# Kernel optimization log

Hardware: AMD Instinct MI355X
Metric: run time of the kernel (lower is better)

Reference implementation:

```python
import jax, jax.numpy as jnp
import numpy as np

PAD = 2  # kernel_height // 2 for kernel_height=5


def earth_pad2d(x, ph, pw):
    # circular pad in longitude (last dim), zero pad in latitude (dim 2)
    if pw > 0:
        x = jnp.concatenate([x[..., -pw:], x, x[..., :pw]], axis=-1)
    if ph > 0:
        x = jnp.pad(x, ((0, 0), (0, 0), (ph, ph), (0, 0)))
    return x


def earth_wrap2d(x, w, pad):
    # fold circular overhang of a transposed-conv output back onto width w
    core = x[..., pad:pad + w]
    rw = x.shape[-1] - pad - w  # right overhang (stride-1... here 1)
    core = core.at[..., :rw].add(x[..., pad + w:])
    core = core.at[..., w - pad:].add(x[..., :pad])
    return core


def _conv(x, w, b, stride):
    # torch Conv2d, weight [Cout, Cin, 1, k], VALID padding, stride (1, stride)
    y = jax.lax.conv_general_dilated(x, w, (1, stride), 'VALID',
                                     dimension_numbers=('NCHW', 'OIHW', 'NCHW'))
    return y + b[None, :, None, None]


def _convT(x, w, stride):
    # torch ConvTranspose2d (no bias), weight [Cin, Cout, 1, k], padding 0
    k = w.shape[-1]
    wr = jnp.transpose(jnp.flip(w, axis=(2, 3)), (1, 0, 2, 3))  # -> [Cout, Cin, 1, k]
    return jax.lax.conv_general_dilated(x, wr, (1, 1),
                                        [(0, 0), (k - 1, k - 1)],
                                        lhs_dilation=(1, stride),
                                        dimension_numbers=('NCHW', 'OIHW', 'NCHW'))


def _edge(x, d, p):
    return x[:, :, -p:, :] if d == 1 else x[:, :, :p, :]


def _set_edge(x, d, p, v):
    return x.at[:, :, -p:, :].set(v) if d == 1 else x.at[:, :, :p, :].set(v)


def _forward(strips, wi, wo):
    strips_pad = [earth_pad2d(s, PAD, PAD) for s in strips]
    # center strip inner edges from the adjacent coarser strips (to_inners[0])
    for d in (-1, 1):
        a = _edge(strips[2 + d], -d, PAD)
        a = _convT(a, wi[0], 2)
        a = earth_wrap2d(a, strips[2].shape[3], 2)
        a = earth_pad2d(a, 0, PAD)
        strips_pad[2] = _set_edge(strips_pad[2], d, PAD, a)
    # outer strips: far edge from next coarser (to_inners), near edge from finer (to_outers)
    for mi in (1, 2):
        for d in (-1, 1):
            idx = 2 + d * mi
            sp = strips_pad[idx]
            if mi + 1 <= 2:
                o = _edge(strips[2 + d * (mi + 1)], -d, PAD)
                o = _convT(o, wi[mi], 2)
                o = earth_wrap2d(o, strips[idx].shape[3], 2)
                o = earth_pad2d(o, 0, PAD)
                sp = _set_edge(sp, d, PAD, o)
            en = _edge(strips[2 + d * (mi - 1)], d, PAD)
            en = earth_pad2d(en, 0, 2)
            en = _conv(en, wo[mi - 1][0], wo[mi - 1][1], 2)
            en = earth_pad2d(en, 0, PAD)
            sp = _set_edge(sp, -d, PAD, en)
            strips_pad[idx] = sp
    return tuple(strips_pad)


def setup_inputs():
    key = jax.random.key(0)
    ks = jax.random.split(key, 11)
    B, C, W = 1, 256, 1440
    shapes = [(B, C, 30, W // 4), (B, C, 60, W // 2), (B, C, 180, W),
              (B, C, 60, W // 2), (B, C, 30, W // 4)]
    d = {}
    for i, sh in enumerate(shapes):
        d['s%d' % i] = jax.random.normal(ks[i], sh, dtype=jnp.float32)
    scale = 0.03
    d['wi0'] = jax.random.normal(ks[5], (C, C, 1, 5), dtype=jnp.float32) * scale
    d['wi1'] = jax.random.normal(ks[6], (C, C, 1, 5), dtype=jnp.float32) * scale
    d['wo0'] = jax.random.normal(ks[7], (C, C, 1, 5), dtype=jnp.float32) * scale
    d['bo0'] = jax.random.normal(ks[8], (C,), dtype=jnp.float32) * 0.01
    d['wo1'] = jax.random.normal(ks[9], (C, C, 1, 5), dtype=jnp.float32) * scale
    d['bo1'] = jax.random.normal(ks[10], (C,), dtype=jnp.float32) * 0.01
    return d


def reference(s0, s1, s2, s3, s4, wi0, wi1, wo0, bo0, wo1, bo1):
    return _forward([s0, s1, s2, s3, s4], [wi0, wi1], [(wo0, bo0), (wo1, bo1)])
```

## Files before the change

kernel.cpp:

```cpp
#include <hip/hip_runtime.h>


struct ConvJob {
  const float* x; const float* wt; const float* bias; float* out;
  int Hin, Win, r0, Hout, Wcore, h0, blk_start;
};

struct MegaParams {
  ConvJob j[8];
  const float* in0; const float* in1; const float* in2; const float* in3; const float* in4;
  float* o0; float* o1; float* o2; float* o3; float* o4;
  unsigned* ctr;
};

struct WTParams { const float* src[4]; float* dst[4]; unsigned* ctr; };

__global__ __launch_bounds__(256) void transpose_all_kernel(WTParams p) {
  if (blockIdx.x == 0 && threadIdx.x == 0) *p.ctr = 0u;
  int b = blockIdx.x;
  int which = b / 1280;
  int idx = (b - which * 1280) * 256 + threadIdx.x;
  int oc = idx & 255;
  int q = idx >> 8;
  int k = q % 5;
  int ic = q / 5;
  const float* s = p.src[which];
  float v = (which < 2) ? s[(ic * 256 + oc) * 5 + k] : s[(oc * 256 + ic) * 5 + k];
  p.dst[which][idx] = v;
}

template <int H, int W>
__device__ __forceinline__ void copy_row(const float* __restrict__ in,
                                         float* __restrict__ out, int rl, int lane) {
  int c = rl / H;
  const float* src = in + (size_t)rl * W;
  float* dst = out + (size_t)(rl + c * 4 + 2) * (W + 4);
  for (int w4 = 1 + lane; w4 < W / 4; w4 += 64) {
    const float* q = src + w4 * 4;
    float2 a = *(const float2*)(q - 2);
    float2 b = *(const float2*)(q);
    *(float4*)(dst + w4 * 4) = make_float4(a.x, a.y, b.x, b.y);
  }
  if (lane == 0) {
    float2 E = *(const float2*)(src + W - 2);
    float2 F = *(const float2*)(src);
    float4 v = make_float4(E.x, E.y, F.x, F.y);
    *(float4*)(dst) = v;
    *(float4*)(dst + W) = v;
  }
}

__device__ __forceinline__ void zero_row(const MegaParams& p, int z, int lane) {
  int strip = z >> 9, cr = z & 511, c = cr >> 1, r = cr & 1;
  float* dst = strip ? p.o4 + (size_t)(c * 34 + 32 + r) * 364
                     : p.o0 + (size_t)(c * 34 + r) * 364;
  for (int w4 = lane; w4 < 91; w4 += 64)
    *(float4*)(dst + w4 * 4) = make_float4(0.f, 0.f, 0.f, 0.f);
}

__device__ __forceinline__ void do_row(const MegaParams& p, int gid, int lane) {
  if (gid < 46080)      copy_row<180, 1440>(p.in2, p.o2, gid, lane);
  else if (gid < 61440) copy_row<60, 720>(p.in1, p.o1, gid - 46080, lane);
  else if (gid < 76800) copy_row<60, 720>(p.in3, p.o3, gid - 61440, lane);
  else if (gid < 84480) copy_row<30, 360>(p.in0, p.o0, gid - 76800, lane);
  else if (gid < 92160) copy_row<30, 360>(p.in4, p.o4, gid - 84480, lane);
  else                  zero_row(p, gid - 92160, lane);
}

__device__ __forceinline__ void conv_tr(const ConvJob jb, int local, int t, float* xs) {
  int tile = local >> 1;
  int r = local & 1;
  const int Win = jb.Win;
  const float* xrow = jb.x + ((size_t)(t * jb.Hin + jb.r0 + r)) * Win;
  const float* wt = jb.wt + t;
  const int Wop = jb.Wcore + 4;
  float* orow = jb.out + ((size_t)(t * jb.Hout + jb.h0 + r)) * Wop;

  int m0 = tile * 16;
  int j0 = (m0 >> 1) - 1;
#pragma unroll
  for (int cc = 0; cc < 10; ++cc) {
    int col = j0 + cc;
    col += (col < 0) ? Win : 0;
    col -= (col >= Win) ? Win : 0;
    xs[cc * 256 + t] = xrow[col];
  }
  __syncthreads();
  float acc[16];
#pragma unroll
  for (int i = 0; i < 16; ++i) acc[i] = 0.f;
  float w[20], wn[20];
#pragma unroll
  for (int e = 0; e < 20; ++e) w[e] = wt[e * 256];
  for (int ic0 = 0; ic0 < 256; ic0 += 4) {
    if (ic0 + 4 < 256) {
#pragma unroll
      for (int e = 0; e < 20; ++e) wn[e] = wt[(size_t)((ic0 + 4) * 5 + e) * 256];
    }
#pragma unroll
    for (int cc = 0; cc < 10; ++cc) {
      float4 xq = *(const float4*)&xs[cc * 256 + ic0];
#pragma unroll
      for (int ml = 0; ml < 16; ++ml) {
        int k = ml + 4 - 2 * cc;
        if (k >= 0 && k < 5)
          acc[ml] += w[k] * xq.x + w[5 + k] * xq.y + w[10 + k] * xq.z + w[15 + k] * xq.w;
      }
    }
#pragma unroll
    for (int e = 0; e < 20; ++e) w[e] = wn[e];
  }
#pragma unroll
  for (int i = 0; i < 16; ++i) {
    int g = m0 + i;
    float vv = acc[i];
    orow[2 + g] = vv;
    if (g < 2) orow[jb.Wcore + 2 + g] = vv;
    if (g >= jb.Wcore - 2) orow[g - (jb.Wcore - 2)] = vv;
  }
}

__device__ __forceinline__ void conv_fwd(const ConvJob jb, int local, int t, float* xs) {
  int tile = local >> 1;
  int r = local & 1;
  const int Win = jb.Win;
  const float* xrow = jb.x + ((size_t)(t * jb.Hin + jb.r0 + r)) * Win;
  const float* wt = jb.wt + t;
  const int Wop = jb.Wcore + 4;
  float* orow = jb.out + ((size_t)(t * jb.Hout + jb.h0 + r)) * Wop;

  int u0 = tile * 8;
  int cb = 2 * u0 - 2;
#pragma unroll
  for (int cc = 0; cc < 19; ++cc) {
    int col = cb + cc;
    col += (col < 0) ? Win : 0;
    col -= (col >= Win) ? Win : 0;
    xs[cc * 256 + t] = xrow[col];
  }
  __syncthreads();
  float bv = jb.bias[t];
  float acc[8];
#pragma unroll
  for (int i = 0; i < 8; ++i) acc[i] = bv;
  float w[20], wn[20];
#pragma unroll
  for (int e = 0; e < 20; ++e) w[e] = wt[e * 256];
  for (int ic0 = 0; ic0 < 256; ic0 += 4) {
    if (ic0 + 4 < 256) {
#pragma unroll
      for (int e = 0; e < 20; ++e) wn[e] = wt[(size_t)((ic0 + 4) * 5 + e) * 256];
    }
#pragma unroll
    for (int cc = 0; cc < 19; ++cc) {
      float4 xq = *(const float4*)&xs[cc * 256 + ic0];
#pragma unroll
      for (int i = 0; i < 8; ++i) {
        int k = cc - 2 * i;
        if (k >= 0 && k < 5)
          acc[i] += w[k] * xq.x + w[5 + k] * xq.y + w[10 + k] * xq.z + w[15 + k] * xq.w;
      }
    }
#pragma unroll
    for (int e = 0; e < 20; ++e) w[e] = wn[e];
  }
#pragma unroll
  for (int i = 0; i < 8; ++i) {
    int g = u0 + i;
    float vv = acc[i];
    orow[2 + g] = vv;
    if (g < 2) orow[jb.Wcore + 2 + g] = vv;
    if (g >= jb.Wcore - 2) orow[g - (jb.Wcore - 2)] = vv;
  }
}

__global__ __launch_bounds__(256, 4) void mega_kernel(MegaParams p) {
  __shared__ float xs[19 * 256];
  int bx = blockIdx.x;
  int t = threadIdx.x;
  if (bx < 540) {
    int ji = (bx >= 450) ? 3 : (bx >= 360) ? 2 : (bx >= 180) ? 1 : 0;
    conv_tr(p.j[ji], bx - p.j[ji].blk_start, t, xs);
    __syncthreads();
    int u2 = bx + 540;
    int j2 = (u2 >= 990) ? 7 : (u2 >= 900) ? 6 : (u2 >= 720) ? 5 : 4;
    conv_fwd(p.j[j2], u2 - p.j[j2].blk_start, t, xs);
  }
  int lane = t & 63;
  for (;;) {
    int g = 0;
    if (lane == 0) g = (int)atomicAdd(p.ctr, 1u);
    g = __shfl(g, 0, 64);
    if (g >= 11648) break;
    int base = g * 8;
    for (int r = 0; r < 8; ++r) do_row(p, base + r, lane);
  }
}

extern "C" void kernel_launch(void* const* d_in, const int* in_sizes, int n_in,
                              void* d_out, int out_size, void* d_ws, size_t ws_size,
                              hipStream_t stream) {
  const float* s0 = (const float*)d_in[0];
  const float* s1 = (const float*)d_in[1];
  const float* s2 = (const float*)d_in[2];
  const float* s3 = (const float*)d_in[3];
  const float* s4 = (const float*)d_in[4];
  const float* wi0 = (const float*)d_in[5];
  const float* wi1 = (const float*)d_in[6];
  const float* wo0 = (const float*)d_in[7];
  const float* bo0 = (const float*)d_in[8];
  const float* wo1 = (const float*)d_in[9];
  const float* bo1 = (const float*)d_in[10];

  float* out = (float*)d_out;
  float* out0 = out;
  float* out1 = out + 3168256;
  float* out2 = out + 15030272;
  float* out3 = out + 83048448;
  float* out4 = out + 94910464;

  unsigned* ctr = (unsigned*)d_ws;
  float* wt0 = (float*)d_ws + 16;
  float* wt1 = wt0 + 327680;
  float* wt2 = wt1 + 327680;
  float* wt3 = wt2 + 327680;

  WTParams wp;
  wp.src[0] = wi0; wp.src[1] = wi1; wp.src[2] = wo0; wp.src[3] = wo1;
  wp.dst[0] = wt0; wp.dst[1] = wt1; wp.dst[2] = wt2; wp.dst[3] = wt3;
  wp.ctr = ctr;
  transpose_all_kernel<<<5120, 256, 0, stream>>>(wp);

  MegaParams mp;
  mp.j[0] = {s1, wt0, nullptr, out2,  60,  720,  58, 184, 1440,   0,   0};
  mp.j[1] = {s3, wt0, nullptr, out2,  60,  720,   0, 184, 1440, 182, 180};
  mp.j[2] = {s0, wt1, nullptr, out1,  30,  360,  28,  64,  720,   0, 360};
  mp.j[3] = {s4, wt1, nullptr, out3,  30,  360,   0,  64,  720,  62, 450};
  mp.j[4] = {s2, wt2, bo0,     out1, 180, 1440,   0,  64,  720,  62, 540};
  mp.j[5] = {s2, wt2, bo0,     out3, 180, 1440, 178,  64,  720,   0, 720};
  mp.j[6] = {s1, wt3, bo1,     out0,  60,  720,   0,  34,  360,  32, 900};
  mp.j[7] = {s3, wt3, bo1,     out4,  60,  720,  58,  34,  360,   0, 990};
  mp.in0 = s0; mp.in1 = s1; mp.in2 = s2; mp.in3 = s3; mp.in4 = s4;
  mp.o0 = out0; mp.o1 = out1; mp.o2 = out2; mp.o3 = out3; mp.o4 = out4;
  mp.ctr = ctr;

  mega_kernel<<<1024, 256, 0, stream>>>(mp);
}
```

Before: 361.8 us.

## Split fused mega-kernel into separate conv and copy kernels with static scheduling

Replaces the single persistent mega-kernel, which ran two conv tiles per block and then pulled copy rows through an atomic counter, with two launches. The conv kernel assigns one conv tile per block across 1080 blocks, and the copy kernel walks rows with a static grid-stride loop. The conv inner loop is restructured into a double-buffered weight load over a non-unrolled loop, and the copy loop is unrolled by two. This removes atomic contention and the serial two-conv chain per block. In exchange it adds a launch and loses the overlap between conv compute and the bandwidth-bound copy inside one kernel.

New measurement: 466.1 us. 1.29x slower.

```diff
diff --git a/kernel.cpp b/kernel.cpp
--- a/kernel.cpp
+++ b/kernel.cpp
@@ -5,18 +5,16 @@
   const float* x; const float* wt; const float* bias; float* out;
   int Hin, Win, r0, Hout, Wcore, h0, blk_start;
 };
-
-struct MegaParams {
-  ConvJob j[8];
+struct ConvParams { ConvJob j[8]; };
+
+struct CopyParams {
   const float* in0; const float* in1; const float* in2; const float* in3; const float* in4;
   float* o0; float* o1; float* o2; float* o3; float* o4;
-  unsigned* ctr;
 };
 
-struct WTParams { const float* src[4]; float* dst[4]; unsigned* ctr; };
+struct WTParams { const float* src[4]; float* dst[4]; };
 
 __global__ __launch_bounds__(256) void transpose_all_kernel(WTParams p) {
-  if (blockIdx.x == 0 && threadIdx.x == 0) *p.ctr = 0u;
   int b = blockIdx.x;
   int which = b / 1280;
   int idx = (b - which * 1280) * 256 + threadIdx.x;
@@ -29,45 +27,30 @@
   p.dst[which][idx] = v;
 }
 
-template <int H, int W>
-__device__ __forceinline__ void copy_row(const float* __restrict__ in,
-                                         float* __restrict__ out, int rl, int lane) {
-  int c = rl / H;
-  const float* src = in + (size_t)rl * W;
-  float* dst = out + (size_t)(rl + c * 4 + 2) * (W + 4);
-  for (int w4 = 1 + lane; w4 < W / 4; w4 += 64) {
-    const float* q = src + w4 * 4;
-    float2 a = *(const float2*)(q - 2);
-    float2 b = *(const float2*)(q);
-    *(float4*)(dst + w4 * 4) = make_float4(a.x, a.y, b.x, b.y);
-  }
-  if (lane == 0) {
-    float2 E = *(const float2*)(src + W - 2);
-    float2 F = *(const float2*)(src);
-    float4 v = make_float4(E.x, E.y, F.x, F.y);
-    *(float4*)(dst) = v;
-    *(float4*)(dst + W) = v;
-  }
-}
-
-__device__ __forceinline__ void zero_row(const MegaParams& p, int z, int lane) {
-  int strip = z >> 9, cr = z & 511, c = cr >> 1, r = cr & 1;
-  float* dst = strip ? p.o4 + (size_t)(c * 34 + 32 + r) * 364
-                     : p.o0 + (size_t)(c * 34 + r) * 364;
-  for (int w4 = lane; w4 < 91; w4 += 64)
-    *(float4*)(dst + w4 * 4) = make_float4(0.f, 0.f, 0.f, 0.f);
-}
-
-__device__ __forceinline__ void do_row(const MegaParams& p, int gid, int lane) {
-  if (gid < 46080)      copy_row<180, 1440>(p.in2, p.o2, gid, lane);
-  else if (gid < 61440) copy_row<60, 720>(p.in1, p.o1, gid - 46080, lane);
-  else if (gid < 76800) copy_row<60, 720>(p.in3, p.o3, gid - 61440, lane);
-  else if (gid < 84480) copy_row<30, 360>(p.in0, p.o0, gid - 76800, lane);
-  else if (gid < 92160) copy_row<30, 360>(p.in4, p.o4, gid - 84480, lane);
-  else                  zero_row(p, gid - 92160, lane);
-}
-
-__device__ __forceinline__ void conv_tr(const ConvJob jb, int local, int t, float* xs) {
+
+template <int NOUT, int NCC>
+__device__ __forceinline__ void fma_cols(float* acc, const float* w, const float* xsrow,
+                                         int ic0) {
+#pragma unroll
+  for (int cc = 0; cc < NCC; ++cc) {
+    float4 xq = *(const float4*)&xsrow[cc * 256 + ic0];
+#pragma unroll
+    for (int i = 0; i < NOUT; ++i) {
+      int k = (NOUT == 8) ? (cc - 2 * i) : (i + 4 - 2 * cc);
+      if (k >= 0 && k < 5)
+        acc[i] += w[k] * xq.x + w[5 + k] * xq.y + w[10 + k] * xq.z + w[15 + k] * xq.w;
+    }
+  }
+}
+
+__device__ __forceinline__ void wload(float* wbuf, const float* wt, int ic) {
+#pragma unroll
+  for (int e = 0; e < 20; ++e) wbuf[e] = wt[(size_t)(ic * 5 + e) * 256];
+}
+
+template <int NOUT, int NCC>
+__device__ __forceinline__ void conv_unit(const ConvJob jb, int local, int t, float* xs,
+                                          float bv) {
   int tile = local >> 1;
   int r = local & 1;
   const int Win = jb.Win;
@@ -76,43 +59,36 @@
   const int Wop = jb.Wcore + 4;
   float* orow = jb.out + ((size_t)(t * jb.Hout + jb.h0 + r)) * Wop;
 
-  int m0 = tile * 16;
-  int j0 = (m0 >> 1) - 1;
-#pragma unroll
-  for (int cc = 0; cc < 10; ++cc) {
-    int col = j0 + cc;
+  int base0, ncc;
+  if (NOUT == 8) { base0 = 2 * (tile * 8) - 2; ncc = 19; }
+  else           { base0 = (tile * 16 >> 1) - 1; ncc = 10; }
+#pragma unroll
+  for (int cc = 0; cc < NCC; ++cc) {
+    int col = base0 + cc;
     col += (col < 0) ? Win : 0;
     col -= (col >= Win) ? Win : 0;
     xs[cc * 256 + t] = xrow[col];
   }
   __syncthreads();
-  float acc[16];
-#pragma unroll
-  for (int i = 0; i < 16; ++i) acc[i] = 0.f;
-  float w[20], wn[20];
-#pragma unroll
-  for (int e = 0; e < 20; ++e) w[e] = wt[e * 256];
-  for (int ic0 = 0; ic0 < 256; ic0 += 4) {
-    if (ic0 + 4 < 256) {
-#pragma unroll
-      for (int e = 0; e < 20; ++e) wn[e] = wt[(size_t)((ic0 + 4) * 5 + e) * 256];
-    }
-#pragma unroll
-    for (int cc = 0; cc < 10; ++cc) {
-      float4 xq = *(const float4*)&xs[cc * 256 + ic0];
-#pragma unroll
-      for (int ml = 0; ml < 16; ++ml) {
-        int k = ml + 4 - 2 * cc;
-        if (k >= 0 && k < 5)
-          acc[ml] += w[k] * xq.x + w[5 + k] * xq.y + w[10 + k] * xq.z + w[15 + k] * xq.w;
-      }
-    }
-#pragma unroll
-    for (int e = 0; e < 20; ++e) w[e] = wn[e];
-  }
-#pragma unroll
-  for (int i = 0; i < 16; ++i) {
-    int g = m0 + i;
+
+  float acc[NOUT];
+#pragma unroll
+  for (int i = 0; i < NOUT; ++i) acc[i] = bv;
+
+  float wA[20], wB[20];
+  wload(wA, wt, 0);
+#pragma unroll 1
+  for (int ic0 = 0; ic0 < 256; ic0 += 8) {
+    wload(wB, wt, ic0 + 4);
+    fma_cols<NOUT, NCC>(acc, wA, xs, ic0);
+    if (ic0 + 8 < 256) wload(wA, wt, ic0 + 8);
+    fma_cols<NOUT, NCC>(acc, wB, xs, ic0 + 4);
+  }
+
+  int g0 = (NOUT == 8) ? tile * 8 : tile * 16;
+#pragma unroll
+  for (int i = 0; i < NOUT; ++i) {
+    int g = g0 + i;
     float vv = acc[i];
     orow[2 + g] = vv;
     if (g < 2) orow[jb.Wcore + 2 + g] = vv;
@@ -120,81 +96,77 @@
   }
 }
 
-__device__ __forceinline__ void conv_fwd(const ConvJob jb, int local, int t, float* xs) {
-  int tile = local >> 1;
-  int r = local & 1;
-  const int Win = jb.Win;
-  const float* xrow = jb.x + ((size_t)(t * jb.Hin + jb.r0 + r)) * Win;
-  const float* wt = jb.wt + t;
-  const int Wop = jb.Wcore + 4;
-  float* orow = jb.out + ((size_t)(t * jb.Hout + jb.h0 + r)) * Wop;
-
-  int u0 = tile * 8;
-  int cb = 2 * u0 - 2;
-#pragma unroll
-  for (int cc = 0; cc < 19; ++cc) {
-    int col = cb + cc;
-    col += (col < 0) ? Win : 0;
-    col -= (col >= Win) ? Win : 0;
-    xs[cc * 256 + t] = xrow[col];
-  }
-  __syncthreads();
-  float bv = jb.bias[t];
-  float acc[8];
-#pragma unroll
-  for (int i = 0; i < 8; ++i) acc[i] = bv;
-  float w[20], wn[20];
-#pragma unroll
-  for (int e = 0; e < 20; ++e) w[e] = wt[e * 256];
-  for (int ic0 = 0; ic0 < 256; ic0 += 4) {
-    if (ic0 + 4 < 256) {
-#pragma unroll
-      for (int e = 0; e < 20; ++e) wn[e] = wt[(size_t)((ic0 + 4) * 5 + e) * 256];
-    }
-#pragma unroll
-    for (int cc = 0; cc < 19; ++cc) {
-      float4 xq = *(const float4*)&xs[cc * 256 + ic0];
-#pragma unroll
-      for (int i = 0; i < 8; ++i) {
-        int k = cc - 2 * i;
-        if (k >= 0 && k < 5)
-          acc[i] += w[k] * xq.x + w[5 + k] * xq.y + w[10 + k] * xq.z + w[15 + k] * xq.w;
-      }
-    }
-#pragma unroll
-    for (int e = 0; e < 20; ++e) w[e] = wn[e];
-  }
-#pragma unroll
-  for (int i = 0; i < 8; ++i) {
-    int g = u0 + i;
-    float vv = acc[i];
-    orow[2 + g] = vv;
-    if (g < 2) orow[jb.Wcore + 2 + g] = vv;
-    if (g >= jb.Wcore - 2) orow[g - (jb.Wcore - 2)] = vv;
-  }
-}
-
-__global__ __launch_bounds__(256, 4) void mega_kernel(MegaParams p) {
+__global__ __launch_bounds__(256, 4) void conv_kernel(ConvParams p) {
   __shared__ float xs[19 * 256];
   int bx = blockIdx.x;
   int t = threadIdx.x;
   if (bx < 540) {
     int ji = (bx >= 450) ? 3 : (bx >= 360) ? 2 : (bx >= 180) ? 1 : 0;
-    conv_tr(p.j[ji], bx - p.j[ji].blk_start, t, xs);
-    __syncthreads();
-    int u2 = bx + 540;
+    conv_unit<16, 10>(p.j[ji], bx - p.j[ji].blk_start, t, xs, 0.f);
+  } else {
+    int u2 = bx;
     int j2 = (u2 >= 990) ? 7 : (u2 >= 900) ? 6 : (u2 >= 720) ? 5 : 4;
-    conv_fwd(p.j[j2], u2 - p.j[j2].blk_start, t, xs);
-  }
-  int lane = t & 63;
-  for (;;) {
-    int g = 0;
-    if (lane == 0) g = (int)atomicAdd(p.ctr, 1u);
-    g = __shfl(g, 0, 64);
-    if (g >= 11648) break;
-    int base = g * 8;
-    for (int r = 0; r < 8; ++r) do_row(p, base + r, lane);
-  }
+    conv_unit<8, 19>(p.j[j2], u2 - p.j[j2].blk_start, t, xs, p.j[j2].bias[t]);
+  }
+}
+
+
+__device__ __forceinline__ float4 pack4(float2 a, float2 b) {
+  return make_float4(a.x, a.y, b.x, b.y);
+}
+
+template <int H, int W>
+__device__ __forceinline__ void copy_row(const float* __restrict__ in,
+                                         float* __restrict__ out, int rl, int lane) {
+  constexpr int CORE = W / 4;
+  int c = rl / H;
+  const float* src = in + (size_t)rl * W;
+  float* dst = out + (size_t)(rl + c * 4 + 2) * (W + 4);
+  int w4 = 1 + lane;
+  while (w4 < CORE) {
+    int w4b = w4 + 64;
+    float2 a0 = *(const float2*)(src + w4 * 4 - 2);
+    float2 b0 = *(const float2*)(src + w4 * 4);
+    if (w4b < CORE) {
+      float2 a1 = *(const float2*)(src + w4b * 4 - 2);
+      float2 b1 = *(const float2*)(src + w4b * 4);
+      *(float4*)(dst + w4 * 4) = pack4(a0, b0);
+      *(float4*)(dst + w4b * 4) = pack4(a1, b1);
+    } else {
+      *(float4*)(dst + w4 * 4) = pack4(a0, b0);
+    }
+    w4 += 128;
+  }
+  if (lane == 0) {
+    float2 E = *(const float2*)(src + W - 2);
+    float2 F = *(const float2*)(src);
+    float4 v = pack4(E, F);
+    *(float4*)(dst) = v;
+    *(float4*)(dst + W) = v;
+  }
+}
+
+__device__ __forceinline__ void zero_row(const CopyParams& p, int z, int lane) {
+  int strip = z >> 9, cr = z & 511, c = cr >> 1, r = cr & 1;
+  float* dst = strip ? p.o4 + (size_t)(c * 34 + 32 + r) * 364
+                     : p.o0 + (size_t)(c * 34 + r) * 364;
+  for (int w4 = lane; w4 < 91; w4 += 64)
+    *(float4*)(dst + w4 * 4) = make_float4(0.f, 0.f, 0.f, 0.f);
+}
+
+__device__ __forceinline__ void do_row(const CopyParams& p, int gid, int lane) {
+  if (gid < 46080)      copy_row<180, 1440>(p.in2, p.o2, gid, lane);
+  else if (gid < 61440) copy_row<60, 720>(p.in1, p.o1, gid - 46080, lane);
+  else if (gid < 76800) copy_row<60, 720>(p.in3, p.o3, gid - 61440, lane);
+  else if (gid < 84480) copy_row<30, 360>(p.in0, p.o0, gid - 76800, lane);
+  else if (gid < 92160) copy_row<30, 360>(p.in4, p.o4, gid - 84480, lane);
+  else                  zero_row(p, gid - 92160, lane);
+}
+
+__global__ __launch_bounds__(256, 8) void copy_kernel(CopyParams p) {
+  int wid = blockIdx.x * 4 + (threadIdx.x >> 6);
+  int lane = threadIdx.x & 63;
+  for (int gid = wid; gid < 93184; gid += 8192) do_row(p, gid, lane);
 }
 
 extern "C" void kernel_launch(void* const* d_in, const int* in_sizes, int n_in,
@@ -219,8 +191,7 @@
   float* out3 = out + 83048448;
   float* out4 = out + 94910464;
 
-  unsigned* ctr = (unsigned*)d_ws;
-  float* wt0 = (float*)d_ws + 16;
+  float* wt0 = (float*)d_ws;
   float* wt1 = wt0 + 327680;
   float* wt2 = wt1 + 327680;
   float* wt3 = wt2 + 327680;
@@ -228,21 +199,21 @@
   WTParams wp;
   wp.src[0] = wi0; wp.src[1] = wi1; wp.src[2] = wo0; wp.src[3] = wo1;
   wp.dst[0] = wt0; wp.dst[1] = wt1; wp.dst[2] = wt2; wp.dst[3] = wt3;
-  wp.ctr = ctr;
   transpose_all_kernel<<<5120, 256, 0, stream>>>(wp);
 
-  MegaParams mp;
-  mp.j[0] = {s1, wt0, nullptr, out2,  60,  720,  58, 184, 1440,   0,   0};
-  mp.j[1] = {s3, wt0, nullptr, out2,  60,  720,   0, 184, 1440, 182, 180};
-  mp.j[2] = {s0, wt1, nullptr, out1,  30,  360,  28,  64,  720,   0, 360};
-  mp.j[3] = {s4, wt1, nullptr, out3,  30,  360,   0,  64,  720,  62, 450};
-  mp.j[4] = {s2, wt2, bo0,     out1, 180, 1440,   0,  64,  720,  62, 540};
-  mp.j[5] = {s2, wt2, bo0,     out3, 180, 1440, 178,  64,  720,   0, 720};
-  mp.j[6] = {s1, wt3, bo1,     out0,  60,  720,   0,  34,  360,  32, 900};
-  mp.j[7] = {s3, wt3, bo1,     out4,  60,  720,  58,  34,  360,   0, 990};
-  mp.in0 = s0; mp.in1 = s1; mp.in2 = s2; mp.in3 = s3; mp.in4 = s4;
-  mp.o0 = out0; mp.o1 = out1; mp.o2 = out2; mp.o3 = out3; mp.o4 = out4;
-  mp.ctr = ctr;
-
-  mega_kernel<<<1024, 256, 0, stream>>>(mp);
-}
+  ConvParams cp;
+  cp.j[0] = {s1, wt0, nullptr, out2,  60,  720,  58, 184, 1440,   0,   0};
+  cp.j[1] = {s3, wt0, nullptr, out2,  60,  720,   0, 184, 1440, 182, 180};
+  cp.j[2] = {s0, wt1, nullptr, out1,  30,  360,  28,  64,  720,   0, 360};
+  cp.j[3] = {s4, wt1, nullptr, out3,  30,  360,   0,  64,  720,  62, 450};
+  cp.j[4] = {s2, wt2, bo0,     out1, 180, 1440,   0,  64,  720,  62, 540};
+  cp.j[5] = {s2, wt2, bo0,     out3, 180, 1440, 178,  64,  720,   0, 720};
+  cp.j[6] = {s1, wt3, bo1,     out0,  60,  720,   0,  34,  360,  32, 900};
+  cp.j[7] = {s3, wt3, bo1,     out4,  60,  720,  58,  34,  360,   0, 990};
+  conv_kernel<<<1080, 256, 0, stream>>>(cp);
+
+  CopyParams kp;
+  kp.in0 = s0; kp.in1 = s1; kp.in2 = s2; kp.in3 = s3; kp.in4 = s4;
+  kp.o0 = out0; kp.o1 = out1; kp.o2 = out2; kp.o3 = out3; kp.o4 = out4;
+  copy_kernel<<<2048, 256, 0, stream>>>(kp);
+}
```
